# Kernel tuning notes

Hardware: AMD Instinct MI355X
Metric: run time of the kernel (lower is better)

The kernel has to match this reference:

```python
import jax, jax.numpy as jnp
import numpy as np

N, DQ, T, H1 = 131072, 256, 4, 512

def setup_inputs() -> dict:
    key = jax.random.key(0)
    k_q, k_w0, k_b0, k_w1, k_z = jax.random.split(key, 5)
    return {
        "q": jax.random.normal(k_q, (N, DQ), dtype=jnp.float32),
        "Z": jax.random.randint(k_z, (N,), 0, T, dtype=jnp.int32),
        "W0": jax.random.normal(k_w0, (T, DQ, H1), dtype=jnp.float32) * (1.0 / np.sqrt(DQ)),
        "b0": jax.random.normal(k_b0, (T, H1), dtype=jnp.float32) * 0.01,
        "W1": jax.random.normal(k_w1, (T, H1), dtype=jnp.float32) * (1.0 / np.sqrt(H1)),
        "b1": jnp.zeros((), dtype=jnp.float32),
    }

def reference(q, Z, W0, b0, W1, b1):
    # Dense grouped-GEMM over all T types (T is small), then select per-atom
    # type result. Avoids materializing the per-atom [N, dq, h1] gathered
    # weight tensor that tf.gather would create.
    h_all = jnp.einsum('nd,tdh->nth', q, W0)              # [N, T, H1]
    h = jnp.take_along_axis(h_all, Z[:, None, None].astype(jnp.int32), axis=1)[:, 0, :]  # [N, H1]
    h = jnp.tanh(h + b0[Z])                               # hidden activations
    F = jnp.einsum('nh,nh->n', h, W1[Z]) + b1             # [N]
    return F
```

## Files before the change

### kernel.cpp

```cpp
#include <hip/hip_runtime.h>
#include <hip/hip_bf16.h>

#define N_ATOMS 131072
#define DQ 256
#define H1 512
#define NTYPES 4
#define TILE_M 64
#define GRID 512

typedef __bf16 bf16x8 __attribute__((ext_vector_type(8)));
typedef float f32x16 __attribute__((ext_vector_type(16)));

__device__ __forceinline__ unsigned short f2bf(float f) {
  unsigned int u = __builtin_bit_cast(unsigned int, f);
  u += 0x7fffu + ((u >> 16) & 1u);
  return (unsigned short)(u >> 16);
}

__device__ __forceinline__ float fast_tanh(float x) {
  float e = __expf(2.0f * x);
  return 1.0f - 2.0f * __builtin_amdgcn_rcpf(e + 1.0f);
}

__global__ __launch_bounds__(64) void init_kernel(int* __restrict__ hdr) {
  if (threadIdx.x < 16) hdr[threadIdx.x] = 0;
}

__global__ __launch_bounds__(256) void prep_kernel(
    const float* __restrict__ W0, const int* __restrict__ Z,
    unsigned short* __restrict__ W0s, int* __restrict__ perm,
    int* __restrict__ cnt)
{
  const int b = blockIdx.x, tid = threadIdx.x;
  const int gid = b * 256 + tid;

  if (gid < NTYPES * (DQ / 8) * H1) {
    const int n  = gid & (H1 - 1);
    const int kg = (gid >> 9) & 31;
    const int t  = gid >> 14;
    const float* src = W0 + ((size_t)(t * DQ + kg * 8) * H1 + n);
    unsigned short o[8];
#pragma unroll
    for (int j = 0; j < 8; ++j) o[j] = f2bf(src[(size_t)j * H1]);
    uint4 v;
    v.x = (unsigned)o[0] | ((unsigned)o[1] << 16);
    v.y = (unsigned)o[2] | ((unsigned)o[3] << 16);
    v.z = (unsigned)o[4] | ((unsigned)o[5] << 16);
    v.w = (unsigned)o[6] | ((unsigned)o[7] << 16);
    ((uint4*)W0s)[gid] = v;
  }

  __shared__ int lc[NTYPES], lbase[NTYPES];
  if (tid < NTYPES) lc[tid] = 0;
  __syncthreads();
  const int t  = Z[gid];
  const int my = atomicAdd(&lc[t], 1);
  __syncthreads();
  if (tid < NTYPES) lbase[tid] = lc[tid] ? atomicAdd(&cnt[tid], lc[tid]) : 0;
  __syncthreads();
  perm[t * N_ATOMS + lbase[t] + my] = gid;
}

__device__ __forceinline__ void issue_half(float4* st, const float* q,
                                           int atom, int c4, int h) {
  const float* p = q + (size_t)atom * DQ + c4 * 64 + h * 32;
#pragma unroll
  for (int i = 0; i < 8; ++i) st[i] = *(const float4*)(p + i * 4);
}

__device__ __forceinline__ void store_half(
    const float4* st, unsigned short (*A)[TILE_M][8], int row, int c4, int h) {
#pragma unroll
  for (int i2 = 0; i2 < 4; ++i2) {
    const int k = c4 * 64 + h * 32 + i2 * 8;
    uint4 vv;
    vv.x = (unsigned)f2bf(st[2*i2].x)   | ((unsigned)f2bf(st[2*i2].y)   << 16);
    vv.y = (unsigned)f2bf(st[2*i2].z)   | ((unsigned)f2bf(st[2*i2].w)   << 16);
    vv.z = (unsigned)f2bf(st[2*i2+1].x) | ((unsigned)f2bf(st[2*i2+1].y) << 16);
    vv.w = (unsigned)f2bf(st[2*i2+1].z) | ((unsigned)f2bf(st[2*i2+1].w) << 16);
    *(uint4*)&A[k >> 3][row][0] = vv;
  }
}

__global__ __launch_bounds__(256, 2) void gemm_persist(
    const float* __restrict__ q, const int* __restrict__ perm,
    const int* __restrict__ cnt,
    const unsigned short* __restrict__ W0s,
    const float* __restrict__ b0g, const float* __restrict__ W1,
    const float* __restrict__ b1p, float* __restrict__ out)
{
  __shared__ unsigned short Alds[2][DQ / 8][TILE_M][8];
  __shared__ float Fws[2][4][TILE_M];

  const int tid = threadIdx.x;
  const int l = tid & 63, w = tid >> 6;
  const int half = l >> 5, ln = l & 31;
  const int row = tid >> 2, c4 = tid & 3;
  const int bx = (int)blockIdx.x;

  const int c0 = cnt[0], c1 = cnt[1], c2 = cnt[2], c3 = cnt[3];
  const int n0 = (c0 + 63) >> 6, n1 = (c1 + 63) >> 6;
  const int n2 = (c2 + 63) >> 6, n3 = (c3 + 63) >> 6;
  const int p1 = n0, p2 = n0 + n1, p3 = n0 + n1 + n2;
  const int total = n0 + n1 + n2 + n3;
  const float b1v = b1p[0];

#define DECODE(v, T, J0, CT) do {                                   \
    T = ((v) >= p1) + ((v) >= p2) + ((v) >= p3);                    \
    const int pre_ = (T == 0) ? 0 : (T == 1) ? p1 : (T == 2) ? p2 : p3; \
    CT = (T == 0) ? c0 : (T == 1) ? c1 : (T == 2) ? c2 : c3;        \
    J0 = ((v) - pre_) * TILE_M; } while (0)

#define EPI_HALF(MT) do {                                                     \
    _Pragma("unroll")                                                         \
    for (int r = 0; r < 16; ++r) {                                            \
      float s = 0.f;                                                          \
      _Pragma("unroll")                                                       \
      for (int nt = 0; nt < 4; ++nt)                                          \
        s += w1v[nt] * fast_tanh(acc[MT][nt][r] + b0v[nt]);                   \
      s += __shfl_xor(s, 1);                                                  \
      s += __shfl_xor(s, 2);                                                  \
      s += __shfl_xor(s, 4);                                                  \
      s += __shfl_xor(s, 8);                                                  \
      s += __shfl_xor(s, 16);                                                 \
      if (ln == 0)                                                            \
        Fws[cur][w][(MT) * 32 + (r & 3) + 8 * (r >> 2) + 4 * half] = s;       \
    }                                                                         \
  } while (0)

  int vt_cur = bx;
  int t_cur, j0_cur, ct_cur;
  DECODE(vt_cur, t_cur, j0_cur, ct_cur);

  float4 st[8];
  {
    int atom = 0;
    if (j0_cur + row < ct_cur) atom = perm[t_cur * N_ATOMS + j0_cur + row];
    issue_half(st, q, atom, c4, 0);
    store_half(st, Alds[0], row, c4, 0);
    issue_half(st, q, atom, c4, 1);
    store_half(st, Alds[0], row, c4, 1);
  }

  int vt_nxt = bx + GRID;
  int t_nxt = 0, j0_nxt = 0, ct_nxt = 0, anext = 0;
  if (vt_nxt < total) {
    DECODE(vt_nxt, t_nxt, j0_nxt, ct_nxt);
    if (j0_nxt + row < ct_nxt) anext = perm[t_nxt * N_ATOMS + j0_nxt + row];
    issue_half(st, q, anext, c4, 0);
  }
  __syncthreads();

  int cur = 0;

  while (vt_cur < total) {
    const bool have_nxt = (vt_nxt < total);

    float b0v[4], w1v[4];
#pragma unroll
    for (int nt = 0; nt < 4; ++nt) {
      const int c = w * 128 + nt * 32 + ln;
      b0v[nt] = b0g[t_cur * H1 + c];
      w1v[nt] = W1[t_cur * H1 + c];
    }

    f32x16 acc[2][4];
#pragma unroll
    for (int mt = 0; mt < 2; ++mt)
#pragma unroll
      for (int nt = 0; nt < 4; ++nt) acc[mt][nt] = (f32x16)0.0f;

    const unsigned short* Bt = W0s + (size_t)t_cur * (DQ * H1);
    const unsigned short* Bbase = Bt + (size_t)(w * 128 + ln) * 8;

    __builtin_amdgcn_s_setprio(1);
#pragma unroll 4
    for (int step = 0; step < 16; ++step) {
      const int kg = 2 * step + half;
      const bf16x8 a0 = *(const bf16x8*)&Alds[cur][kg][ln][0];
      const bf16x8 a1 = *(const bf16x8*)&Alds[cur][kg][32 + ln][0];
      const unsigned short* bptr = Bbase + (size_t)kg * (H1 * 8);
      const bf16x8 b0f = *(const bf16x8*)(bptr);
      const bf16x8 b1f = *(const bf16x8*)(bptr + 32 * 8);
      const bf16x8 b2f = *(const bf16x8*)(bptr + 64 * 8);
      const bf16x8 b3f = *(const bf16x8*)(bptr + 96 * 8);
      acc[0][0] = __builtin_amdgcn_mfma_f32_32x32x16_bf16(a0, b0f, acc[0][0], 0, 0, 0);
      acc[1][0] = __builtin_amdgcn_mfma_f32_32x32x16_bf16(a1, b0f, acc[1][0], 0, 0, 0);
      acc[0][1] = __builtin_amdgcn_mfma_f32_32x32x16_bf16(a0, b1f, acc[0][1], 0, 0, 0);
      acc[1][1] = __builtin_amdgcn_mfma_f32_32x32x16_bf16(a1, b1f, acc[1][1], 0, 0, 0);
      acc[0][2] = __builtin_amdgcn_mfma_f32_32x32x16_bf16(a0, b2f, acc[0][2], 0, 0, 0);
      acc[1][2] = __builtin_amdgcn_mfma_f32_32x32x16_bf16(a1, b2f, acc[1][2], 0, 0, 0);
      acc[0][3] = __builtin_amdgcn_mfma_f32_32x32x16_bf16(a0, b3f, acc[0][3], 0, 0, 0);
      acc[1][3] = __builtin_amdgcn_mfma_f32_32x32x16_bf16(a1, b3f, acc[1][3], 0, 0, 0);
    }
    __builtin_amdgcn_s_setprio(0);

    if (have_nxt) store_half(st, Alds[cur ^ 1], row, c4, 0);

    if (have_nxt) issue_half(st, q, anext, c4, 1);

    EPI_HALF(0);
    EPI_HALF(1);

    if (have_nxt) store_half(st, Alds[cur ^ 1], row, c4, 1);

    __syncthreads();

    if (tid < TILE_M && j0_cur + tid < ct_cur) {
      const int a = perm[t_cur * N_ATOMS + j0_cur + tid];
      out[a] = Fws[cur][0][tid] + Fws[cur][1][tid] + Fws[cur][2][tid]
             + Fws[cur][3][tid] + b1v;
    }

    vt_cur = vt_nxt;
    if (have_nxt) {
      t_cur = t_nxt; j0_cur = j0_nxt; ct_cur = ct_nxt;
      vt_nxt += GRID;
      anext = 0;
      if (vt_nxt < total) {
        DECODE(vt_nxt, t_nxt, j0_nxt, ct_nxt);
        if (j0_nxt + row < ct_nxt) anext = perm[t_nxt * N_ATOMS + j0_nxt + row];
        issue_half(st, q, anext, c4, 0);
      }
    }
    cur ^= 1;
  }
#undef DECODE
#undef EPI_HALF
}

extern "C" void kernel_launch(void* const* d_in, const int* in_sizes, int n_in,
                              void* d_out, int out_size, void* d_ws, size_t ws_size,
                              hipStream_t stream) {
  const float* q  = (const float*)d_in[0];
  const int*   Z  = (const int*)d_in[1];
  const float* W0 = (const float*)d_in[2];
  const float* b0 = (const float*)d_in[3];
  const float* W1 = (const float*)d_in[4];
  const float* b1 = (const float*)d_in[5];
  float* out = (float*)d_out;

  char* ws = (char*)d_ws;
  int* hdr    = (int*)(ws);
  int* cnt    = hdr;
  int* perm   = (int*)(ws + 64);
  unsigned short* W0s =
      (unsigned short*)(ws + 64 + (size_t)NTYPES * N_ATOMS * 4);

  hipLaunchKernelGGL(init_kernel, dim3(1), dim3(64), 0, stream, hdr);
  hipLaunchKernelGGL(prep_kernel, dim3(512), dim3(256), 0, stream,
                     W0, Z, W0s, perm, cnt);
  hipLaunchKernelGGL(gemm_persist, dim3(GRID), dim3(256), 0, stream,
                     q, perm, cnt, W0s, b0, W1, b1, out);
}
```

Before: 275.1 us.

## Split ragged per-type tail tiles across blocks and drop bounds checks

Only full 64-row tiles now go through the persistent loop, which removes the per-row bounds checks there. The leftover partial tile of each type is handled by the first 32 blocks, each computing a 64-column slice and combining results with atomicAdd into an output that the init kernel now zeroes. This targets the tail where a few blocks would otherwise process one extra full tile. The next-tile q prefetch is also moved after the MFMA loop, interleaved with the epilogue, along with the b0/W1 loads. In exchange there are atomics, a larger init kernel that writes the whole output, and extra work for the first 32 blocks.

```diff
diff --git a/kernel.cpp b/kernel.cpp
--- a/kernel.cpp
+++ b/kernel.cpp
@@ -22,8 +22,11 @@
   return 1.0f - 2.0f * __builtin_amdgcn_rcpf(e + 1.0f);
 }
 
-__global__ __launch_bounds__(64) void init_kernel(int* __restrict__ hdr) {
-  if (threadIdx.x < 16) hdr[threadIdx.x] = 0;
+__global__ __launch_bounds__(256) void init_kernel(int* __restrict__ hdr,
+                                                   float* __restrict__ out) {
+  const int gid = blockIdx.x * 256 + threadIdx.x;
+  if (gid < 16) hdr[gid] = 0;
+  for (int i = gid; i < N_ATOMS; i += 512 * 256) out[i] = 0.0f;
 }
 
 __global__ __launch_bounds__(256) void prep_kernel(
@@ -99,16 +102,14 @@
   const int bx = (int)blockIdx.x;
 
   const int c0 = cnt[0], c1 = cnt[1], c2 = cnt[2], c3 = cnt[3];
-  const int n0 = (c0 + 63) >> 6, n1 = (c1 + 63) >> 6;
-  const int n2 = (c2 + 63) >> 6, n3 = (c3 + 63) >> 6;
-  const int p1 = n0, p2 = n0 + n1, p3 = n0 + n1 + n2;
-  const int total = n0 + n1 + n2 + n3;
+  const int n0f = c0 >> 6, n1f = c1 >> 6, n2f = c2 >> 6, n3f = c3 >> 6;
+  const int p1 = n0f, p2 = n0f + n1f, p3 = n0f + n1f + n2f;
+  const int total = n0f + n1f + n2f + n3f;
   const float b1v = b1p[0];
 
-#define DECODE(v, T, J0, CT) do {                                   \
+#define DECODE(v, T, J0) do {                                       \
     T = ((v) >= p1) + ((v) >= p2) + ((v) >= p3);                    \
     const int pre_ = (T == 0) ? 0 : (T == 1) ? p1 : (T == 2) ? p2 : p3; \
-    CT = (T == 0) ? c0 : (T == 1) ? c1 : (T == 2) ? c2 : c3;        \
     J0 = ((v) - pre_) * TILE_M; } while (0)
 
 #define EPI_HALF(MT) do {                                                     \
@@ -128,42 +129,91 @@
     }                                                                         \
   } while (0)
 
+  if (bx < 32) {
+    const int pr = bx >> 3, cg = bx & 7;
+    int tt = -1, seen = 0;
+#pragma unroll
+    for (int t = 0; t < NTYPES; ++t) {
+      const int ct_ = (t == 0) ? c0 : (t == 1) ? c1 : (t == 2) ? c2 : c3;
+      if (ct_ & 63) { if (seen == pr) tt = t; ++seen; }
+    }
+    if (tt >= 0) {
+      const int ct  = (tt == 0) ? c0 : (tt == 1) ? c1 : (tt == 2) ? c2 : c3;
+      const int base = ct & ~63;
+      {
+        const int aj = base + row;
+        const int atom = perm[tt * N_ATOMS + ((aj < ct) ? aj : base)];
+        float4 st[8];
+        issue_half(st, q, atom, c4, 0);
+        store_half(st, Alds[0], row, c4, 0);
+        issue_half(st, q, atom, c4, 1);
+        store_half(st, Alds[0], row, c4, 1);
+      }
+      __syncthreads();
+
+      const int rowgrp = w & 1, colgrp = w >> 1;
+      const int col = cg * 64 + colgrp * 32 + ln;
+      const unsigned short* Bt = W0s + (size_t)tt * (DQ * H1);
+      const unsigned short* Bbase = Bt + (size_t)col * 8;
+
+      f32x16 acc1 = (f32x16)0.0f;
+#pragma unroll 4
+      for (int step = 0; step < 16; ++step) {
+        const int kg = 2 * step + half;
+        const bf16x8 a = *(const bf16x8*)&Alds[0][kg][rowgrp * 32 + ln][0];
+        const bf16x8 bfr = *(const bf16x8*)(Bbase + (size_t)kg * (H1 * 8));
+        acc1 = __builtin_amdgcn_mfma_f32_32x32x16_bf16(a, bfr, acc1, 0, 0, 0);
+      }
+
+      const float b0v1 = b0g[tt * H1 + col];
+      const float w1v1 = W1[tt * H1 + col];
+#pragma unroll
+      for (int r = 0; r < 16; ++r) {
+        float s = w1v1 * fast_tanh(acc1[r] + b0v1);
+        s += __shfl_xor(s, 1);
+        s += __shfl_xor(s, 2);
+        s += __shfl_xor(s, 4);
+        s += __shfl_xor(s, 8);
+        s += __shfl_xor(s, 16);
+        if (ln == 0)
+          Fws[0][colgrp][rowgrp * 32 + (r & 3) + 8 * (r >> 2) + 4 * half] = s;
+      }
+      __syncthreads();
+
+      if (tid < TILE_M) {
+        const int aj = base + tid;
+        if (aj < ct) {
+          const float part = Fws[0][0][tid] + Fws[0][1][tid]
+                           + ((cg == 0) ? b1v : 0.0f);
+          atomicAdd(&out[perm[tt * N_ATOMS + aj]], part);
+        }
+      }
+    }
+  }
+
   int vt_cur = bx;
-  int t_cur, j0_cur, ct_cur;
-  DECODE(vt_cur, t_cur, j0_cur, ct_cur);
+  int t_cur, j0_cur;
+  DECODE(vt_cur, t_cur, j0_cur);
 
   float4 st[8];
   {
-    int atom = 0;
-    if (j0_cur + row < ct_cur) atom = perm[t_cur * N_ATOMS + j0_cur + row];
+    const int atom = perm[t_cur * N_ATOMS + j0_cur + row];
     issue_half(st, q, atom, c4, 0);
     store_half(st, Alds[0], row, c4, 0);
     issue_half(st, q, atom, c4, 1);
     store_half(st, Alds[0], row, c4, 1);
   }
+  __syncthreads();
 
   int vt_nxt = bx + GRID;
-  int t_nxt = 0, j0_nxt = 0, ct_nxt = 0, anext = 0;
+  int t_nxt = 0, j0_nxt = 0, anext = 0;
   if (vt_nxt < total) {
-    DECODE(vt_nxt, t_nxt, j0_nxt, ct_nxt);
-    if (j0_nxt + row < ct_nxt) anext = perm[t_nxt * N_ATOMS + j0_nxt + row];
-    issue_half(st, q, anext, c4, 0);
-  }
-  __syncthreads();
-
+    DECODE(vt_nxt, t_nxt, j0_nxt);
+    anext = perm[t_nxt * N_ATOMS + j0_nxt + row];
+  }
   int cur = 0;
 
   while (vt_cur < total) {
-    const bool have_nxt = (vt_nxt < total);
-
-    float b0v[4], w1v[4];
-#pragma unroll
-    for (int nt = 0; nt < 4; ++nt) {
-      const int c = w * 128 + nt * 32 + ln;
-      b0v[nt] = b0g[t_cur * H1 + c];
-      w1v[nt] = W1[t_cur * H1 + c];
-    }
-
     f32x16 acc[2][4];
 #pragma unroll
     for (int mt = 0; mt < 2; ++mt)
@@ -195,18 +245,27 @@
     }
     __builtin_amdgcn_s_setprio(0);
 
+    const bool have_nxt = (vt_nxt < total);
+
+    float b0v[4], w1v[4];
+#pragma unroll
+    for (int nt = 0; nt < 4; ++nt) {
+      const int c = w * 128 + nt * 32 + ln;
+      b0v[nt] = b0g[t_cur * H1 + c];
+      w1v[nt] = W1[t_cur * H1 + c];
+    }
+
+    if (have_nxt) issue_half(st, q, anext, c4, 0);
+    EPI_HALF(0);
     if (have_nxt) store_half(st, Alds[cur ^ 1], row, c4, 0);
 
     if (have_nxt) issue_half(st, q, anext, c4, 1);
-
-    EPI_HALF(0);
     EPI_HALF(1);
-
     if (have_nxt) store_half(st, Alds[cur ^ 1], row, c4, 1);
 
     __syncthreads();
 
-    if (tid < TILE_M && j0_cur + tid < ct_cur) {
+    if (tid < TILE_M) {
       const int a = perm[t_cur * N_ATOMS + j0_cur + tid];
       out[a] = Fws[cur][0][tid] + Fws[cur][1][tid] + Fws[cur][2][tid]
              + Fws[cur][3][tid] + b1v;
@@ -214,13 +273,11 @@
 
     vt_cur = vt_nxt;
     if (have_nxt) {
-      t_cur = t_nxt; j0_cur = j0_nxt; ct_cur = ct_nxt;
+      t_cur = t_nxt; j0_cur = j0_nxt;
       vt_nxt += GRID;
-      anext = 0;
       if (vt_nxt < total) {
-        DECODE(vt_nxt, t_nxt, j0_nxt, ct_nxt);
-        if (j0_nxt + row < ct_nxt) anext = perm[t_nxt * N_ATOMS + j0_nxt + row];
-        issue_half(st, q, anext, c4, 0);
+        DECODE(vt_nxt, t_nxt, j0_nxt);
+        anext = perm[t_nxt * N_ATOMS + j0_nxt + row];
       }
     }
     cur ^= 1;
@@ -247,7 +304,7 @@
   unsigned short* W0s =
       (unsigned short*)(ws + 64 + (size_t)NTYPES * N_ATOMS * 4);
 
-  hipLaunchKernelGGL(init_kernel, dim3(1), dim3(64), 0, stream, hdr);
+  hipLaunchKernelGGL(init_kernel, dim3(512), dim3(256), 0, stream, hdr, out);
   hipLaunchKernelGGL(prep_kernel, dim3(512), dim3(256), 0, stream,
                      W0, Z, W0s, perm, cnt);
   hipLaunchKernelGGL(gemm_persist, dim3(GRID), dim3(256), 0, stream,
```

After: 270.0 us. About the same (-1.8%).
